# Performance work log

Hardware: AMD Instinct MI355X
Metric: run time of the kernel (lower is better)

## Reference

```python
import jax, jax.numpy as jnp
import numpy as np

B, T_SUB, L, H, K = 64, 512, 256, 1024, 9


def setup_inputs() -> dict:
    key = jax.random.key(0)
    ks = jax.random.split(key, 8)
    sequence_output = jax.random.normal(ks[0], (B, T_SUB, H), jnp.float32)
    attention_mask = jnp.ones((B, T_SUB), jnp.int32)
    offsets = jnp.sort(jax.random.randint(ks[1], (B, L), 0, T_SUB), axis=1)
    mask = jnp.ones((B, L), bool)
    labels = jax.random.randint(ks[2], (B, L), 0, K)
    classifier_w = jax.random.normal(ks[3], (H, K), jnp.float32) / np.sqrt(H).astype(np.float32)
    classifier_b = jnp.zeros((K,), jnp.float32)
    start_transitions = jax.random.uniform(ks[4], (K,), jnp.float32, -0.1, 0.1)
    end_transitions = jax.random.uniform(ks[5], (K,), jnp.float32, -0.1, 0.1)
    transitions = jax.random.uniform(ks[6], (K, K), jnp.float32, -0.1, 0.1)
    return {
        'sequence_output': sequence_output, 'attention_mask': attention_mask,
        'offsets': offsets, 'mask': mask, 'labels': labels,
        'classifier_w': classifier_w, 'classifier_b': classifier_b,
        'start_transitions': start_transitions, 'end_transitions': end_transitions,
        'transitions': transitions,
    }


def crf_log_likelihood(emissions, tags, mask_b, start, trans, end):
    # emissions [B,L,K], tags [B,L] int, mask_b [B,L] bool (mask[:,0] all True)
    maskf = mask_b.astype(emissions.dtype)
    # numerator: score of the gold path
    first_tag = tags[:, 0]
    score = start[first_tag] + jnp.take_along_axis(emissions[:, 0], first_tag[:, None], 1)[:, 0]
    trans_sc = trans[tags[:, :-1], tags[:, 1:]]                                   # [B,L-1]
    emit_sc = jnp.take_along_axis(emissions[:, 1:], tags[:, 1:, None], 2)[..., 0]  # [B,L-1]
    score = score + jnp.sum((trans_sc + emit_sc) * maskf[:, 1:], axis=1)
    seq_ends = jnp.sum(mask_b.astype(jnp.int32), axis=1) - 1
    last_tags = jnp.take_along_axis(tags, seq_ends[:, None], 1)[:, 0]
    score = score + end[last_tags]
    # denominator: log partition via scan over time
    def step(alpha, xs):
        em_i, m_i = xs  # [B,K], [B]
        nxt = jax.nn.logsumexp(alpha[:, :, None] + trans[None] + em_i[:, None, :], axis=1)
        return jnp.where(m_i[:, None], nxt, alpha), None
    alpha0 = start[None] + emissions[:, 0]
    xs = (jnp.swapaxes(emissions[:, 1:], 0, 1), jnp.swapaxes(mask_b[:, 1:], 0, 1))
    alphaL, _ = jax.lax.scan(step, alpha0, xs)
    denom = jax.nn.logsumexp(alphaL + end[None], axis=1)
    return score - denom


def crf_viterbi(emissions, mask_b, start, trans, end):
    k = emissions.shape[-1]
    iden = jnp.arange(k)[None, :]
    def step(score, xs):
        em_i, m_i = xs
        cand = score[:, :, None] + trans[None]     # [B,K_prev,K_cur]
        idx = jnp.argmax(cand, axis=1)             # [B,K]
        nxt = jnp.max(cand, axis=1) + em_i
        score = jnp.where(m_i[:, None], nxt, score)
        idx = jnp.where(m_i[:, None], idx, iden)   # identity through padding
        return score, idx
    score0 = start[None] + emissions[:, 0]
    xs = (jnp.swapaxes(emissions[:, 1:], 0, 1), jnp.swapaxes(mask_b[:, 1:], 0, 1))
    final, hist = jax.lax.scan(step, score0, xs)   # hist [L-1,B,K]
    last = jnp.argmax(final + end[None], axis=1)   # [B]
    def back(tag, h):
        prev = jnp.take_along_axis(h, tag[:, None], 1)[:, 0]
        return prev, tag
    tag0, ys = jax.lax.scan(back, last, hist, reverse=True)  # ys[i] = tag_{i+1}
    path = jnp.concatenate([tag0[None], ys], axis=0)          # [L,B]
    return jnp.swapaxes(path, 0, 1)


def reference(sequence_output, attention_mask, offsets, mask, labels,
              classifier_w, classifier_b, start_transitions, end_transitions, transitions):
    # embedder: sub_token_mode='first' -> gather first-subtoken embedding per word
    embed = jnp.take_along_axis(sequence_output, offsets[:, :, None], axis=1)  # [B,L,H]
    # dropout is identity at inference
    logits = embed @ classifier_w + classifier_b                               # [B,L,K]
    crf_mask = mask                                                            # word-level CRF mask
    tags = labels * crf_mask.astype(labels.dtype)
    llh = crf_log_likelihood(logits, tags, crf_mask, start_transitions, transitions, end_transitions)
    loss = -jnp.mean(llh)
    predicts = crf_viterbi(logits, crf_mask, start_transitions, transitions, end_transitions)
    predicts = predicts * crf_mask.astype(predicts.dtype)
    return loss, logits, predicts
```

## Files before the change

### kernel.cpp

```cpp
#include <hip/hip_runtime.h>
#include <hip/hip_bf16.h>
#include <math.h>

#define BB 64
#define TSUB 512
#define LL 256
#define HH 1024
#define KK 9

#define S_CHUNK 37
#define N_CHUNK 7

__device__ __forceinline__ float bcast(float v, int lane) {
    return __int_as_float(__builtin_amdgcn_readlane(__float_as_int(v), lane));
}
__device__ __forceinline__ float fexp2(float x) { return __builtin_amdgcn_exp2f(x); }
__device__ __forceinline__ float flog2(float x) { return __builtin_amdgcn_logf(x); }

__global__ __launch_bounds__(256) void logits_kernel(
    const float* __restrict__ seq,
    const int*   __restrict__ offsets,
    const float* __restrict__ w,
    const float* __restrict__ bias,
    float*       __restrict__ logits)
{
    __shared__ float w_s[KK][HH];
    const int tid = threadIdx.x;

    for (int i = tid; i < HH * KK; i += 256) {
        int h = i / KK, k = i - h * KK;
        w_s[k][h] = w[i];
    }
    __syncthreads();

    const int wave = tid >> 6;
    const int lane = tid & 63;
    const int r_local = lane >> 2;
    const int s = lane & 3;

    const int row = blockIdx.x * 64 + wave * 16 + r_local;
    const int b = row >> 8;
    const int l = row & 255;
    const int off = offsets[b * LL + l];
    const float* __restrict__ src = seq + ((size_t)(b * TSUB + off)) * HH;

    float acc[KK];
#pragma unroll
    for (int k = 0; k < KK; ++k) acc[k] = 0.0f;

#pragma unroll 4
    for (int i = 0; i < 64; ++i) {
        const int h0 = i * 16 + s * 4;
        float4 x = *(const float4*)(src + h0);
#pragma unroll
        for (int k = 0; k < KK; ++k) {
            float4 wv = *(const float4*)&w_s[k][h0];
            acc[k] += x.x * wv.x + x.y * wv.y + x.z * wv.z + x.w * wv.w;
        }
    }

#pragma unroll
    for (int k = 0; k < KK; ++k) {
        float v = acc[k];
        v += __shfl_xor(v, 1, 64);
        v += __shfl_xor(v, 2, 64);
        acc[k] = v;
    }

    if (s == 0) {
#pragma unroll
        for (int k = 0; k < KK; ++k)
            logits[(size_t)row * KK + k] = acc[k] + bias[k];
    }
}

__global__ __launch_bounds__(256) void crf_kernel(
    const float* __restrict__ logits,
    const int*   __restrict__ labels,
    const float* __restrict__ start_t,
    const float* __restrict__ end_t,
    const float* __restrict__ trans,
    float*       __restrict__ predicts,
    float*       __restrict__ llh_ws)
{
    __shared__ float em2[LL * KK];
    __shared__ int   lab[LL];
    __shared__ int   hist[(LL - 1) * KK];
    __shared__ int   path[LL];
    __shared__ float s_trans[KK * KK];
    __shared__ int   Fmap[N_CHUNK * KK];
    __shared__ int   s_bnd[N_CHUNK + 1];
    __shared__ float s_denom, s_score;

    const float LOG2E = 1.4426950408889634f;
    const float LN2   = 0.6931471805599453f;

    const int b = blockIdx.x;
    const int tid = threadIdx.x;
    const float* __restrict__ base = logits + (size_t)b * LL * KK;

    for (int i = tid; i < LL * KK; i += 256)
        em2[i] = base[i] * LOG2E;
    for (int i = tid; i < LL; i += 256)
        lab[i] = labels[b * LL + i];
    if (tid < KK * KK) s_trans[tid] = trans[tid];
    __syncthreads();

    const int wave = tid >> 6;
    const int lane = tid & 63;
    const int j = (lane < KK) ? lane : 0;

    if (wave == 0) {
        float tcol2[KK], dt2[KK];
#pragma unroll
        for (int i = 0; i < KK; ++i) tcol2[i] = trans[i * KK + j] * LOG2E;
#pragma unroll
        for (int i = 1; i < KK; ++i) dt2[i] = tcol2[i] - tcol2[0];
        const float endj2 = end_t[j] * LOG2E;

        float a2 = start_t[j] * LOG2E + em2[j];
        float emv = em2[KK + j];
        for (int t = 1; t < LL; ++t) {
            float em_cur = emv;
            if (t + 1 < LL) emv = em2[(t + 1) * KK + j];
            float sa0 = bcast(a2, 0);
            float d = a2 - sa0;
            float q[KK];
#pragma unroll
            for (int i = 1; i < KK; ++i) q[i] = bcast(d, i) + dt2[i];
            float e1 = fexp2(q[1]), e2 = fexp2(q[2]);
            float e3 = fexp2(q[3]), e4 = fexp2(q[4]);
            float e5 = fexp2(q[5]), e6 = fexp2(q[6]);
            float e7 = fexp2(q[7]), e8 = fexp2(q[8]);
            float sum = (((e1 + e2) + (e3 + e4)) + ((e5 + e6) + (e7 + e8))) + 1.0f;
            a2 = sa0 + tcol2[0] + flog2(sum) + em_cur;
        }
        float v = a2 + endj2;
        float c[KK];
#pragma unroll
        for (int i = 0; i < KK; ++i) c[i] = bcast(v, i);
        float m = c[0];
#pragma unroll
        for (int i = 1; i < KK; ++i) m = fmaxf(m, c[i]);
        float sum = 0.0f;
#pragma unroll
        for (int i = 0; i < KK; ++i) sum += fexp2(c[i] - m);
        if (lane == 0) s_denom = (m + flog2(sum)) * LN2;
    } else if (wave == 1) {
        float tcol2[KK];
#pragma unroll
        for (int i = 0; i < KK; ++i) tcol2[i] = trans[i * KK + j] * LOG2E;
        const float endj2 = end_t[j] * LOG2E;

        float vs = start_t[j] * LOG2E + em2[j];
        float emv = em2[KK + j];
        for (int t = 1; t < LL; ++t) {
            float em_cur = emv;
            if (t + 1 < LL) emv = em2[(t + 1) * KK + j];
            float cand[KK];
#pragma unroll
            for (int i = 0; i < KK; ++i) cand[i] = bcast(vs, i) + tcol2[i];
            float m = fmaxf(fmaxf(fmaxf(cand[0], cand[1]), cand[2]),
                     fmaxf(fmaxf(fmaxf(cand[3], cand[4]), cand[5]),
                           fmaxf(fmaxf(cand[6], cand[7]), cand[8])));
            vs = m + em_cur;
            int bi = KK - 1;
#pragma unroll
            for (int i = KK - 2; i >= 0; --i) bi = (cand[i] == m) ? i : bi;
            hist[(t - 1) * KK + j] = bi;
        }
        float v = vs + endj2;
        float c[KK];
#pragma unroll
        for (int i = 0; i < KK; ++i) c[i] = bcast(v, i);
        float bv = c[0];
        int last = 0;
#pragma unroll
        for (int i = 1; i < KK; ++i) { if (c[i] > bv) { bv = c[i]; last = i; } }

        if (lane < N_CHUNK * KK) {
            const int cid = lane / KK;
            const int jj  = lane - cid * KK;
            const int lo = cid * S_CHUNK;
            int hi = lo + S_CHUNK;
            if (hi > LL - 1) hi = LL - 1;
            hi -= 1;
            int f = jj;
            for (int r = hi; r >= lo; --r) f = hist[r * KK + f];
            Fmap[cid * KK + jj] = f;
        }
        if (lane == 0) {
            s_bnd[N_CHUNK] = last;
            int st = last;
            for (int c2 = N_CHUNK - 1; c2 >= 0; --c2) {
                st = Fmap[c2 * KK + st];
                s_bnd[c2] = st;
            }
        }
        if (lane < N_CHUNK) {
            const int lo = lane * S_CHUNK;
            int hi = lo + S_CHUNK;
            if (hi > LL - 1) hi = LL - 1;
            hi -= 1;
            int x = s_bnd[lane + 1];
            for (int r = hi; r >= lo; --r) {
                x = hist[r * KK + x];
                path[r] = x;
            }
        }
        if (lane == 0) path[LL - 1] = last;
    } else if (wave == 2) {
        float part = 0.0f;
        for (int t = 1 + lane; t < LL; t += 64) {
            int tp = lab[t - 1], tc = lab[t];
            part += s_trans[tp * KK + tc] + base[t * KK + tc];
        }
#pragma unroll
        for (int d = 32; d; d >>= 1) part += __shfl_xor(part, d, 64);
        if (lane == 0) {
            int t0 = lab[0], tl = lab[LL - 1];
            s_score = part + start_t[t0] + base[t0] + end_t[tl];
        }
    }
    __syncthreads();

    for (int i = tid; i < LL; i += 256)
        predicts[b * LL + i] = (float)path[i];
    if (tid == 0) llh_ws[b] = s_score - s_denom;
}

__global__ void loss_kernel(const float* __restrict__ llh_ws,
                            float* __restrict__ out)
{
    const int lane = threadIdx.x;
    float v = llh_ws[lane];
#pragma unroll
    for (int d = 32; d; d >>= 1) v += __shfl_xor(v, d, 64);
    if (lane == 0) out[0] = -v / (float)BB;
}

extern "C" void kernel_launch(void* const* d_in, const int* in_sizes, int n_in,
                              void* d_out, int out_size, void* d_ws, size_t ws_size,
                              hipStream_t stream)
{
    (void)in_sizes; (void)n_in; (void)out_size; (void)ws_size;

    const float* seq     = (const float*)d_in[0];
    const int*   offsets = (const int*)d_in[2];
    const int*   labels  = (const int*)d_in[4];
    const float* w       = (const float*)d_in[5];
    const float* bias    = (const float*)d_in[6];
    const float* start_t = (const float*)d_in[7];
    const float* end_t   = (const float*)d_in[8];
    const float* trans   = (const float*)d_in[9];

    float* out      = (float*)d_out;
    float* logits   = out + 1;
    float* predicts = out + 1 + BB * LL * KK;
    float* llh_ws   = (float*)d_ws;

    logits_kernel<<<(BB * LL) / 64, 256, 0, stream>>>(seq, offsets, w, bias, logits);
    crf_kernel<<<BB, 256, 0, stream>>>(logits, labels, start_t, end_t, trans,
                                       predicts, llh_ws);
    loss_kernel<<<1, 64, 0, stream>>>(llh_ws, out);
}
```

Measured before the change: 260.0 us.

## Split logits GEMV across H quarters and fuse loss reduction into CRF kernel

The logits kernel now splits the hidden dimension into four quarters, launching four times as many blocks with a quarter-sized shared weight tile, and writes partial sums to workspace. The CRF kernel sums the partials plus bias, writes the logits, and computes the gold-path score from shared memory. A last-block atomic counter replaces the separate loss kernel. This is meant to raise occupancy and parallelism in the gather-GEMV and drop one launch, at the cost of extra partial-sum traffic and atomic synchronisation.

```diff
diff --git a/kernel.cpp b/kernel.cpp
--- a/kernel.cpp
+++ b/kernel.cpp
@@ -11,25 +11,34 @@
 #define S_CHUNK 37
 #define N_CHUNK 7
 
+#define HQ 256
+#define NQ 4
+#define P_STRIDE (BB * LL * KK)
+
 __device__ __forceinline__ float bcast(float v, int lane) {
     return __int_as_float(__builtin_amdgcn_readlane(__float_as_int(v), lane));
 }
 __device__ __forceinline__ float fexp2(float x) { return __builtin_amdgcn_exp2f(x); }
 __device__ __forceinline__ float flog2(float x) { return __builtin_amdgcn_logf(x); }
 
-__global__ __launch_bounds__(256) void logits_kernel(
+__global__ __launch_bounds__(256) void logits_part_kernel(
     const float* __restrict__ seq,
     const int*   __restrict__ offsets,
     const float* __restrict__ w,
-    const float* __restrict__ bias,
-    float*       __restrict__ logits)
+    float*       __restrict__ part,
+    int*         __restrict__ counter)
 {
-    __shared__ float w_s[KK][HH];
+    if (blockIdx.x == 0 && threadIdx.x == 0)
+        __hip_atomic_store(counter, 0, __ATOMIC_RELAXED, __HIP_MEMORY_SCOPE_AGENT);
+
+    __shared__ float w_s[KK][HQ];
     const int tid = threadIdx.x;
-
-    for (int i = tid; i < HH * KK; i += 256) {
+    const int q     = blockIdx.x & 3;
+    const int group = blockIdx.x >> 2;
+
+    for (int i = tid; i < HQ * KK; i += 256) {
         int h = i / KK, k = i - h * KK;
-        w_s[k][h] = w[i];
+        w_s[k][h] = w[q * (HQ * KK) + i];
     }
     __syncthreads();
 
@@ -38,18 +47,19 @@
     const int r_local = lane >> 2;
     const int s = lane & 3;
 
-    const int row = blockIdx.x * 64 + wave * 16 + r_local;
+    const int row = group * 64 + wave * 16 + r_local;
     const int b = row >> 8;
     const int l = row & 255;
     const int off = offsets[b * LL + l];
-    const float* __restrict__ src = seq + ((size_t)(b * TSUB + off)) * HH;
+    const float* __restrict__ src =
+        seq + ((size_t)(b * TSUB + off)) * HH + q * HQ;
 
     float acc[KK];
 #pragma unroll
     for (int k = 0; k < KK; ++k) acc[k] = 0.0f;
 
 #pragma unroll 4
-    for (int i = 0; i < 64; ++i) {
+    for (int i = 0; i < HQ / 16; ++i) {
         const int h0 = i * 16 + s * 4;
         float4 x = *(const float4*)(src + h0);
 #pragma unroll
@@ -70,18 +80,22 @@
     if (s == 0) {
 #pragma unroll
         for (int k = 0; k < KK; ++k)
-            logits[(size_t)row * KK + k] = acc[k] + bias[k];
+            part[(size_t)q * P_STRIDE + (size_t)row * KK + k] = acc[k];
     }
 }
 
 __global__ __launch_bounds__(256) void crf_kernel(
-    const float* __restrict__ logits,
+    const float* __restrict__ part,
     const int*   __restrict__ labels,
+    const float* __restrict__ bias,
     const float* __restrict__ start_t,
     const float* __restrict__ end_t,
     const float* __restrict__ trans,
+    float*       __restrict__ loss_out,
+    float*       __restrict__ logits,
     float*       __restrict__ predicts,
-    float*       __restrict__ llh_ws)
+    float*       __restrict__ llh_ws,
+    int*         __restrict__ counter)
 {
     __shared__ float em2[LL * KK];
     __shared__ int   lab[LL];
@@ -91,16 +105,24 @@
     __shared__ int   Fmap[N_CHUNK * KK];
     __shared__ int   s_bnd[N_CHUNK + 1];
     __shared__ float s_denom, s_score;
+    __shared__ int   s_last;
 
     const float LOG2E = 1.4426950408889634f;
     const float LN2   = 0.6931471805599453f;
 
     const int b = blockIdx.x;
     const int tid = threadIdx.x;
-    const float* __restrict__ base = logits + (size_t)b * LL * KK;
-
-    for (int i = tid; i < LL * KK; i += 256)
-        em2[i] = base[i] * LOG2E;
+    const size_t base_off = (size_t)b * LL * KK;
+
+    for (int i = tid; i < LL * KK; i += 256) {
+        int k = i % KK;
+        float v = part[base_off + i] +
+                  part[P_STRIDE + base_off + i] +
+                  part[2 * (size_t)P_STRIDE + base_off + i] +
+                  part[3 * (size_t)P_STRIDE + base_off + i] + bias[k];
+        logits[base_off + i] = v;
+        em2[i] = v * LOG2E;
+    }
     for (int i = tid; i < LL; i += 256)
         lab[i] = labels[b * LL + i];
     if (tid < KK * KK) s_trans[tid] = trans[tid];
@@ -210,33 +232,39 @@
         }
         if (lane == 0) path[LL - 1] = last;
     } else if (wave == 2) {
-        float part = 0.0f;
+        float part_s = 0.0f;
         for (int t = 1 + lane; t < LL; t += 64) {
             int tp = lab[t - 1], tc = lab[t];
-            part += s_trans[tp * KK + tc] + base[t * KK + tc];
-        }
-#pragma unroll
-        for (int d = 32; d; d >>= 1) part += __shfl_xor(part, d, 64);
+            part_s += s_trans[tp * KK + tc] + em2[t * KK + tc] * LN2;
+        }
+#pragma unroll
+        for (int d = 32; d; d >>= 1) part_s += __shfl_xor(part_s, d, 64);
         if (lane == 0) {
             int t0 = lab[0], tl = lab[LL - 1];
-            s_score = part + start_t[t0] + base[t0] + end_t[tl];
+            s_score = part_s + start_t[t0] + em2[t0] * LN2 + end_t[tl];
         }
     }
     __syncthreads();
 
     for (int i = tid; i < LL; i += 256)
         predicts[b * LL + i] = (float)path[i];
-    if (tid == 0) llh_ws[b] = s_score - s_denom;
-}
-
-__global__ void loss_kernel(const float* __restrict__ llh_ws,
-                            float* __restrict__ out)
-{
-    const int lane = threadIdx.x;
-    float v = llh_ws[lane];
-#pragma unroll
-    for (int d = 32; d; d >>= 1) v += __shfl_xor(v, d, 64);
-    if (lane == 0) out[0] = -v / (float)BB;
+
+    if (tid == 0) {
+        float llh = s_score - s_denom;
+        __hip_atomic_store(&llh_ws[b], llh, __ATOMIC_RELEASE,
+                           __HIP_MEMORY_SCOPE_AGENT);
+        int old = __hip_atomic_fetch_add(counter, 1, __ATOMIC_ACQ_REL,
+                                         __HIP_MEMORY_SCOPE_AGENT);
+        s_last = (old == BB - 1) ? 1 : 0;
+    }
+    __syncthreads();
+    if (s_last && wave == 0) {
+        float v = __hip_atomic_load(&llh_ws[lane], __ATOMIC_ACQUIRE,
+                                    __HIP_MEMORY_SCOPE_AGENT);
+#pragma unroll
+        for (int d = 32; d; d >>= 1) v += __shfl_xor(v, d, 64);
+        if (lane == 0) loss_out[0] = -v / (float)BB;
+    }
 }
 
 extern "C" void kernel_launch(void* const* d_in, const int* in_sizes, int n_in,
@@ -257,10 +285,14 @@
     float* out      = (float*)d_out;
     float* logits   = out + 1;
     float* predicts = out + 1 + BB * LL * KK;
-    float* llh_ws   = (float*)d_ws;
-
-    logits_kernel<<<(BB * LL) / 64, 256, 0, stream>>>(seq, offsets, w, bias, logits);
-    crf_kernel<<<BB, 256, 0, stream>>>(logits, labels, start_t, end_t, trans,
-                                       predicts, llh_ws);
-    loss_kernel<<<1, 64, 0, stream>>>(llh_ws, out);
-}
+
+    float* part    = (float*)d_ws;
+    float* llh_ws  = part + (size_t)NQ * P_STRIDE;
+    int*   counter = (int*)(llh_ws + BB + 16);
+
+    logits_part_kernel<<<(BB * LL / 64) * NQ, 256, 0, stream>>>(
+        seq, offsets, w, part, counter);
+    crf_kernel<<<BB, 256, 0, stream>>>(part, labels, bias, start_t, end_t,
+                                       trans, out, logits, predicts,
+                                       llh_ws, counter);
+}
```

Measured after the change: 235.8 us. 9.3% less time.
